# Performance work log

Measured on AMD Instinct MI355X. Metric: run time of the kernel, lower is better.

## Reference

```python
import jax, jax.numpy as jnp
import numpy as np

MIN_RANGE, MAX_RANGE = -128.0, 127.0
B, S, F_IN, F_OUT = 4, 2048, 4096, 4096
ROUNDS, FACTOR = 12, 2  # 4096 = 2**12 -> 12 prime factors of 2
NBLK = F_IN // FACTOR   # 2048 blocks of 2x2 per round


def setup_inputs() -> dict:
    key = jax.random.key(0)
    ks = jax.random.split(key, 5)
    x = jax.random.normal(ks[0], (B, S, F_IN), jnp.float32)
    weight = jax.random.normal(ks[1], (F_OUT, F_IN), jnp.float32) * (1.0 / np.sqrt(F_IN))
    bias = jax.random.normal(ks[2], (F_OUT,), jnp.float32)
    perm_keys = jax.random.split(ks[3], ROUNDS)
    permutations = jnp.stack([jax.random.permutation(k, F_IN) for k in perm_keys])  # (ROUNDS, F_IN) int32
    # random 2x2 orthogonal blocks via batched QR (stand-in for ortho_group.rvs)
    a = jax.random.normal(ks[4], (ROUNDS, NBLK, FACTOR, FACTOR), jnp.float32)
    matrices, _ = jnp.linalg.qr(a)  # (ROUNDS, NBLK, FACTOR, FACTOR)
    return {"x": x, "weight": weight, "bias": bias,
            "matrices": matrices, "permutations": permutations}


def _rotate(v, permutations, matrices):
    # v: (..., F_IN). Each round: permute features, then block-diagonal orthogonal matmul.
    for r in range(ROUNDS):
        v = v[..., permutations[r]]
        lead = v.shape[:-1]
        vb = v.reshape(lead + (NBLK, FACTOR))
        vb = jnp.einsum('kij,...kj->...ki', matrices[r], vb)
        v = vb.reshape(lead + (F_IN,))
    return v


def _quant_dequant(t):
    # per-tensor asymmetric quantization to [MIN_RANGE, MAX_RANGE] then dequant
    lo = t.min()
    hi = t.max()
    scale = (hi - lo) / (MAX_RANGE - MIN_RANGE)
    q = jnp.clip(jnp.round((t - lo) / scale) + MIN_RANGE, MIN_RANGE, MAX_RANGE)
    return (q - MIN_RANGE) * scale + lo


def reference(x, weight, bias, matrices, permutations):
    # permuted_x = permute_op(x.mT).mT  <=>  rotate along the feature (last) dim
    x_rot = _rotate(x, permutations, matrices)          # (B, S, F_IN)
    # permuted_weight = permute_op(W.mT, inv_mT).mT; for orthogonal blocks inv.mT == M
    w_rot = _rotate(weight, permutations, matrices)     # (F_OUT, F_IN)
    xq = _quant_dequant(x_rot)
    wq = _quant_dequant(w_rot)
    return jnp.einsum('bsf,of->bso', xq, wq) + bias     # (B, S, F_OUT)
```

## Files before the change

kernel.cpp:

```cpp
#include <hip/hip_runtime.h>

#define F_DIM  4096
#define NROUNDS 12
#define GM     8192
#define GN     4096
#define GK     4096
#define BK2    128
#define NIT2   (GK / BK2)

typedef int  int4v __attribute__((ext_vector_type(4)));
typedef signed char schar;

typedef __attribute__((address_space(3))) void lds_void;
typedef const __attribute__((address_space(1))) void glob_void;

__device__ __forceinline__ unsigned ordf(float f) {
    unsigned u = __float_as_uint(f);
    return (u & 0x80000000u) ? ~u : (u | 0x80000000u);
}
__device__ __forceinline__ float unordf(unsigned u) {
    unsigned v = (u & 0x80000000u) ? (u & 0x7fffffffu) : ~u;
    return __uint_as_float(v);
}

__global__ void init_mm_kernel(unsigned* mm) {
    if (threadIdx.x < 4) mm[threadIdx.x] = (threadIdx.x & 1) ? 0u : 0xFFFFFFFFu;
}

__global__ __launch_bounds__(256)
void rotate_store_kernel(const float* __restrict__ xsrc,
                         const float* __restrict__ wsrc,
                         const int*   __restrict__ perms,
                         const float* __restrict__ mats,
                         unsigned*    __restrict__ mm,
                         float*       __restrict__ xdst,
                         float*       __restrict__ wdst)
{
    __shared__ float4 buf[F_DIM];
    const int t = threadIdx.x;
    const int b = blockIdx.x;
    const bool isW = b < (GN / 4);
    const float* __restrict__ src = isW ? wsrc : xsrc;
    float* __restrict__ dst = isW ? wdst : xdst;
    unsigned* mmp = mm + (isW ? 2 : 0);
    const size_t r0 = (size_t)(isW ? b : b - GN / 4) * 4;

    const int2*   pbase = (const int2*)perms;
    const float4* mbase = (const float4*)mats;

    const float2* s0 = (const float2*)(src + (r0 + 0) * F_DIM);
    const float2* s1 = (const float2*)(src + (r0 + 1) * F_DIM);
    const float2* s2 = (const float2*)(src + (r0 + 2) * F_DIM);
    const float2* s3 = (const float2*)(src + (r0 + 3) * F_DIM);
    #pragma unroll
    for (int q = 0; q < 8; ++q) {
        const int e = t + q * 256;
        float2 a = s0[e], b2 = s1[e], c = s2[e], d = s3[e];
        buf[e]        = make_float4(a.x, b2.x, c.x, d.x);
        buf[e + 2048] = make_float4(a.y, b2.y, c.y, d.y);
    }
    __syncthreads();

    int2 pA[8], pB[8];
    float4 mA[8], mB[8];
    #pragma unroll
    for (int q = 0; q < 8; ++q) { int k = t + q * 256; pA[q] = pbase[k]; mA[q] = mbase[k]; }

    #pragma unroll 1
    for (int r = 0; r < 10; r += 2) {
        float4 va[8], vb[8];
        #pragma unroll
        for (int q = 0; q < 8; ++q) {
            int fa = pA[q].x, fb = pA[q].y;
            va[q] = buf[(fa >> 1) + ((fa & 1) << 11)];
            vb[q] = buf[(fb >> 1) + ((fb & 1) << 11)];
        }
        {
            const int2*   pr = pbase + (size_t)(r + 1) * 2048;
            const float4* mr = mbase + (size_t)(r + 1) * 2048;
            #pragma unroll
            for (int q = 0; q < 8; ++q) { int k = t + q * 256; pB[q] = pr[k]; mB[q] = mr[k]; }
        }
        __syncthreads();
        #pragma unroll
        for (int q = 0; q < 8; ++q) {
            const int k = t + q * 256;
            float4 A = va[q], B = vb[q], M = mA[q];
            buf[k]        = make_float4(M.x*A.x + M.y*B.x, M.x*A.y + M.y*B.y,
                                        M.x*A.z + M.y*B.z, M.x*A.w + M.y*B.w);
            buf[k + 2048] = make_float4(M.z*A.x + M.w*B.x, M.z*A.y + M.w*B.y,
                                        M.z*A.z + M.w*B.z, M.z*A.w + M.w*B.w);
        }
        __syncthreads();

        #pragma unroll
        for (int q = 0; q < 8; ++q) {
            int fa = pB[q].x, fb = pB[q].y;
            va[q] = buf[(fa >> 1) + ((fa & 1) << 11)];
            vb[q] = buf[(fb >> 1) + ((fb & 1) << 11)];
        }
        {
            const int2*   pr = pbase + (size_t)(r + 2) * 2048;
            const float4* mr = mbase + (size_t)(r + 2) * 2048;
            #pragma unroll
            for (int q = 0; q < 8; ++q) { int k = t + q * 256; pA[q] = pr[k]; mA[q] = mr[k]; }
        }
        __syncthreads();
        #pragma unroll
        for (int q = 0; q < 8; ++q) {
            const int k = t + q * 256;
            float4 A = va[q], B = vb[q], M = mB[q];
            buf[k]        = make_float4(M.x*A.x + M.y*B.x, M.x*A.y + M.y*B.y,
                                        M.x*A.z + M.y*B.z, M.x*A.w + M.y*B.w);
            buf[k + 2048] = make_float4(M.z*A.x + M.w*B.x, M.z*A.y + M.w*B.y,
                                        M.z*A.z + M.w*B.z, M.z*A.w + M.w*B.w);
        }
        __syncthreads();
    }

    {
        float4 va[8], vb[8];
        #pragma unroll
        for (int q = 0; q < 8; ++q) {
            int fa = pA[q].x, fb = pA[q].y;
            va[q] = buf[(fa >> 1) + ((fa & 1) << 11)];
            vb[q] = buf[(fb >> 1) + ((fb & 1) << 11)];
        }
        {
            const int2*   pr = pbase + (size_t)11 * 2048;
            const float4* mr = mbase + (size_t)11 * 2048;
            #pragma unroll
            for (int q = 0; q < 8; ++q) { int k = t + q * 256; pB[q] = pr[k]; mB[q] = mr[k]; }
        }
        __syncthreads();
        #pragma unroll
        for (int q = 0; q < 8; ++q) {
            const int k = t + q * 256;
            float4 A = va[q], B = vb[q], M = mA[q];
            buf[k]        = make_float4(M.x*A.x + M.y*B.x, M.x*A.y + M.y*B.y,
                                        M.x*A.z + M.y*B.z, M.x*A.w + M.y*B.w);
            buf[k + 2048] = make_float4(M.z*A.x + M.w*B.x, M.z*A.y + M.w*B.y,
                                        M.z*A.z + M.w*B.z, M.z*A.w + M.w*B.w);
        }
        __syncthreads();
    }

    float lmin = __FLT_MAX__, lmax = -__FLT_MAX__;
    {
        float4 va[8], vb[8];
        #pragma unroll
        for (int q = 0; q < 8; ++q) {
            int fa = pB[q].x, fb = pB[q].y;
            va[q] = buf[(fa >> 1) + ((fa & 1) << 11)];
            vb[q] = buf[(fb >> 1) + ((fb & 1) << 11)];
        }
        #pragma unroll
        for (int q = 0; q < 8; ++q) {
            const int e = t + q * 256;
            float4 A = va[q], B = vb[q], M = mB[q];
            float4 f0 = make_float4(M.x*A.x + M.y*B.x, M.x*A.y + M.y*B.y,
                                    M.x*A.z + M.y*B.z, M.x*A.w + M.y*B.w);
            float4 f1 = make_float4(M.z*A.x + M.w*B.x, M.z*A.y + M.w*B.y,
                                    M.z*A.z + M.w*B.z, M.z*A.w + M.w*B.w);
            lmin = fminf(lmin, fminf(fminf(f0.x, f0.y), fminf(f0.z, f0.w)));
            lmin = fminf(lmin, fminf(fminf(f1.x, f1.y), fminf(f1.z, f1.w)));
            lmax = fmaxf(lmax, fmaxf(fmaxf(f0.x, f0.y), fmaxf(f0.z, f0.w)));
            lmax = fmaxf(lmax, fmaxf(fmaxf(f1.x, f1.y), fmaxf(f1.z, f1.w)));
            ((float2*)(dst + (r0 + 0) * F_DIM))[e] = make_float2(f0.x, f1.x);
            ((float2*)(dst + (r0 + 1) * F_DIM))[e] = make_float2(f0.y, f1.y);
            ((float2*)(dst + (r0 + 2) * F_DIM))[e] = make_float2(f0.z, f1.z);
            ((float2*)(dst + (r0 + 3) * F_DIM))[e] = make_float2(f0.w, f1.w);
        }
    }
    #pragma unroll
    for (int off = 32; off > 0; off >>= 1) {
        lmin = fminf(lmin, __shfl_down(lmin, off));
        lmax = fmaxf(lmax, __shfl_down(lmax, off));
    }
    if ((t & 63) == 0) {
        atomicMin(&mmp[0], ordf(lmin));
        atomicMax(&mmp[1], ordf(lmax));
    }
}

__global__ __launch_bounds__(256)
void quant_row_kernel(const float* __restrict__ src,
                      schar*       __restrict__ dst,
                      int*         __restrict__ rowsum,
                      const unsigned* __restrict__ mm, int sel)
{
    const int row = blockIdx.x, t = threadIdx.x;
    const float lo = unordf(mm[sel]);
    const float hi = unordf(mm[sel + 1]);
    const float scale = (hi - lo) / 255.0f;
    const float4* s = (const float4*)(src + (size_t)row * F_DIM);
    unsigned* d = (unsigned*)(dst + (size_t)row * F_DIM);
    int sum = 0;
    #pragma unroll
    for (int j = 0; j < 4; ++j) {
        const int c = t + 256 * j;
        float4 v = s[c];
        int p0 = (int)fminf(fmaxf(rintf((v.x - lo) / scale), 0.0f), 255.0f);
        int p1 = (int)fminf(fmaxf(rintf((v.y - lo) / scale), 0.0f), 255.0f);
        int p2 = (int)fminf(fmaxf(rintf((v.z - lo) / scale), 0.0f), 255.0f);
        int p3 = (int)fminf(fmaxf(rintf((v.w - lo) / scale), 0.0f), 255.0f);
        sum += p0 + p1 + p2 + p3 - 512;
        unsigned pack = ((unsigned)(p0 - 128) & 0xffu)
                      | (((unsigned)(p1 - 128) & 0xffu) << 8)
                      | (((unsigned)(p2 - 128) & 0xffu) << 16)
                      | (((unsigned)(p3 - 128) & 0xffu) << 24);
        d[c] = pack;
    }
    #pragma unroll
    for (int off = 32; off > 0; off >>= 1) sum += __shfl_down(sum, off);
    __shared__ int part[4];
    if ((t & 63) == 0) part[t >> 6] = sum;
    __syncthreads();
    if (t == 0) rowsum[row] = part[0] + part[1] + part[2] + part[3];
}

__global__ __launch_bounds__(256)
void gemm_i8_bias_kernel(const schar* __restrict__ A,
                         const schar* __restrict__ B,
                         const float* __restrict__ bias,
                         const int*   __restrict__ Rx,
                         const int*   __restrict__ Rw,
                         const unsigned* __restrict__ mm,
                         float*       __restrict__ C)
{
    __shared__ alignas(16) schar As[128 * 8 * 16];
    __shared__ alignas(16) schar Bs[128 * 8 * 16];
    const int t = threadIdx.x;
    const int bid = blockIdx.x;
    const int mb = (bid >> 8) * 8 + (bid & 7);
    const int nb = (bid >> 3) & 31;
    const int lane = t & 63, wv = t >> 6;
    const int wm = (wv & 1) * 64, wn = (wv >> 1) * 64;
    const int rr = lane & 15, kc = lane >> 4;

    const int srow = t >> 3;
    const int cg   = (t & 7) ^ (srow & 7);
    const schar* pa = A + ((size_t)(mb * 128 + srow) * GK) + cg * 16;
    const schar* pb = B + ((size_t)(nb * 128 + srow) * GK) + cg * 16;

    int4v acc[4][4];
    const int4v zz = {0, 0, 0, 0};
    #pragma unroll
    for (int mi = 0; mi < 4; ++mi)
        #pragma unroll
        for (int ni = 0; ni < 4; ++ni)
            acc[mi][ni] = zz;

    auto stage = [&](int k0) {
        #pragma unroll
        for (int j = 0; j < 4; ++j) {
            __builtin_amdgcn_global_load_lds(
                (glob_void*)(pa + (size_t)j * 32 * GK + k0),
                (lds_void*)&As[(size_t)(wv * 64 + 256 * j) * 16], 16, 0, 0);
            __builtin_amdgcn_global_load_lds(
                (glob_void*)(pb + (size_t)j * 32 * GK + k0),
                (lds_void*)&Bs[(size_t)(wv * 64 + 256 * j) * 16], 16, 0, 0);
        }
    };

    stage(0);
    #pragma unroll 1
    for (int it = 0; it < NIT2; ++it) {
        __syncthreads();

        int4v af[2][4], bfr[2][4];
        #pragma unroll
        for (int kk = 0; kk < 2; ++kk) {
            #pragma unroll
            for (int mi = 0; mi < 4; ++mi)
                af[kk][mi] = *(const int4v*)
                    &As[(size_t)((wm + mi * 16 + rr) * 8 + ((kk * 4 + kc) ^ (rr & 7))) * 16];
            #pragma unroll
            for (int ni = 0; ni < 4; ++ni)
                bfr[kk][ni] = *(const int4v*)
                    &Bs[(size_t)((wn + ni * 16 + rr) * 8 + ((kk * 4 + kc) ^ (rr & 7))) * 16];
        }
        __syncthreads();

        if (it + 1 < NIT2) stage((it + 1) * BK2);

        #pragma unroll
        for (int kk = 0; kk < 2; ++kk)
            #pragma unroll
            for (int mi = 0; mi < 4; ++mi)
                #pragma unroll
                for (int ni = 0; ni < 4; ++ni)
                    acc[mi][ni] = __builtin_amdgcn_mfma_i32_16x16x64_i8(
                        af[kk][mi], bfr[kk][ni], acc[mi][ni], 0, 0, 0);
    }

    const float lox = unordf(mm[0]), hix = unordf(mm[1]);
    const float low = unordf(mm[2]), hiw = unordf(mm[3]);
    const float ax = (hix - lox) / 255.0f, aw = (hiw - low) / 255.0f;
    const float cx = 128.0f * ax + lox, cw = 128.0f * aw + low;
    const float sxw = ax * aw;
    const float kcc = (float)GK * cx * cw;
    const float axcw = ax * cw, awcx = aw * cx;

    float colt[4];
    #pragma unroll
    for (int ni = 0; ni < 4; ++ni) {
        const int col = nb * 128 + wn + ni * 16 + rr;
        colt[ni] = awcx * (float)Rw[col] + kcc + bias[col];
    }
    float rowt[4][4];
    #pragma unroll
    for (int mi = 0; mi < 4; ++mi)
        #pragma unroll
        for (int r = 0; r < 4; ++r)
            rowt[mi][r] = axcw * (float)Rx[mb * 128 + wm + mi * 16 + kc * 4 + r];

    #pragma unroll
    for (int mi = 0; mi < 4; ++mi) {
        #pragma unroll
        for (int ni = 0; ni < 4; ++ni) {
            const int col = nb * 128 + wn + ni * 16 + rr;
            #pragma unroll
            for (int r = 0; r < 4; ++r) {
                const int row = mb * 128 + wm + mi * 16 + kc * 4 + r;
                C[(size_t)row * GN + col] =
                    sxw * (float)acc[mi][ni][r] + rowt[mi][r] + colt[ni];
            }
        }
    }
}

extern "C" void kernel_launch(void* const* d_in, const int* in_sizes, int n_in,
                              void* d_out, int out_size, void* d_ws, size_t ws_size,
                              hipStream_t stream)
{
    (void)in_sizes; (void)n_in; (void)out_size; (void)ws_size;
    const float* x     = (const float*)d_in[0];
    const float* w     = (const float*)d_in[1];
    const float* bias  = (const float*)d_in[2];
    const float* mats  = (const float*)d_in[3];
    const int*   perms = (const int*)d_in[4];
    float* out = (float*)d_out;

    char* ws = (char*)d_ws;
    float*    wrot = (float*)ws;
    schar*    xq8  = (schar*)ws;
    int*      Rx   = (int*)(ws + (size_t)32 * 1024 * 1024);
    schar*    wq8  = (schar*)(ws + (size_t)64 * 1024 * 1024);
    int*      Rw   = (int*)(ws + (size_t)80 * 1024 * 1024);
    unsigned* mm   = (unsigned*)(ws + (size_t)81 * 1024 * 1024);
    float*    xrot = out;

    init_mm_kernel<<<1, 64, 0, stream>>>(mm);
    rotate_store_kernel<<<GN / 4 + GM / 4, 256, 0, stream>>>(
        x, w, perms, mats, mm, xrot, wrot);
    quant_row_kernel<<<GN, 256, 0, stream>>>(wrot, wq8, Rw, mm, 2);
    quant_row_kernel<<<GM, 256, 0, stream>>>(xrot, xq8, Rx, mm, 0);
    gemm_i8_bias_kernel<<<GM / 128 * GN / 128, 256, 0, stream>>>(
        xq8, wq8, bias, Rx, Rw, mm, out);
}
```

Before: 703.7 us.

## Fuse pairs of rotation rounds via precomputed composite gather metadata

A new small kernel precomputes, for each pair of rotation rounds, the four composed source indices and the selected coefficients of the first round's 2x2 blocks. The rotate kernel then applies two rounds per LDS pass: it gathers four float4 values, does two chained 2x2 mixes in registers, and stores once. This halves the number of LDS write/barrier phases, from 12 round passes to 6. It costs an extra kernel launch, more gather reads and more registers per pass, and adds a launch_bounds minimum of 2 blocks per SM.

```diff
diff --git a/kernel.cpp b/kernel.cpp
--- a/kernel.cpp
+++ b/kernel.cpp
@@ -28,10 +28,43 @@
 }
 
 __global__ __launch_bounds__(256)
+void fuse_meta_kernel(const int*   __restrict__ perms,
+                      const float* __restrict__ mats,
+                      int4v*  __restrict__ fidx,
+                      float4* __restrict__ fmaC,
+                      float4* __restrict__ fm2)
+{
+    const int g = blockIdx.x * 256 + threadIdx.x;
+    if (g >= 6 * 2048) return;
+    const int rp = g >> 11, j = g & 2047;
+    const int r0 = 2 * rp, r1 = 2 * rp + 1;
+    const int a = perms[r1 * 4096 + 2 * j];
+    const int b = perms[r1 * 4096 + 2 * j + 1];
+    const int i0 = perms[r0 * 4096 + 2 * (a >> 1)];
+    const int i1 = perms[r0 * 4096 + 2 * (a >> 1) + 1];
+    const int i2 = perms[r0 * 4096 + 2 * (b >> 1)];
+    const int i3 = perms[r0 * 4096 + 2 * (b >> 1) + 1];
+    const float4 Ma = ((const float4*)mats)[r0 * 2048 + (a >> 1)];
+    const float4 Mb = ((const float4*)mats)[r0 * 2048 + (b >> 1)];
+    float4 mc;
+    mc.x = (a & 1) ? Ma.z : Ma.x;  mc.y = (a & 1) ? Ma.w : Ma.y;
+    mc.z = (b & 1) ? Mb.z : Mb.x;  mc.w = (b & 1) ? Mb.w : Mb.y;
+    int4v s;
+    s[0] = (i0 >> 1) + ((i0 & 1) << 11);
+    s[1] = (i1 >> 1) + ((i1 & 1) << 11);
+    s[2] = (i2 >> 1) + ((i2 & 1) << 11);
+    s[3] = (i3 >> 1) + ((i3 & 1) << 11);
+    fidx[g] = s;
+    fmaC[g] = mc;
+    fm2[g]  = ((const float4*)mats)[r1 * 2048 + j];
+}
+
+__global__ __launch_bounds__(256, 2)
 void rotate_store_kernel(const float* __restrict__ xsrc,
                          const float* __restrict__ wsrc,
-                         const int*   __restrict__ perms,
-                         const float* __restrict__ mats,
+                         const int4v*  __restrict__ fidx,
+                         const float4* __restrict__ fmaC,
+                         const float4* __restrict__ fm2,
                          unsigned*    __restrict__ mm,
                          float*       __restrict__ xdst,
                          float*       __restrict__ wdst)
@@ -45,9 +78,6 @@
     unsigned* mmp = mm + (isW ? 2 : 0);
     const size_t r0 = (size_t)(isW ? b : b - GN / 4) * 4;
 
-    const int2*   pbase = (const int2*)perms;
-    const float4* mbase = (const float4*)mats;
-
     const float2* s0 = (const float2*)(src + (r0 + 0) * F_DIM);
     const float2* s1 = (const float2*)(src + (r0 + 1) * F_DIM);
     const float2* s2 = (const float2*)(src + (r0 + 2) * F_DIM);
@@ -61,116 +91,141 @@
     }
     __syncthreads();
 
-    int2 pA[8], pB[8];
-    float4 mA[8], mB[8];
-    #pragma unroll
-    for (int q = 0; q < 8; ++q) { int k = t + q * 256; pA[q] = pbase[k]; mA[q] = mbase[k]; }
+    int4v  iA[8], iB[8];
+    float4 aA[8], aB[8], mA[8], mB[8];
+    #pragma unroll
+    for (int q = 0; q < 8; ++q) {
+        int k = t + q * 256;
+        iA[q] = fidx[k]; aA[q] = fmaC[k]; mA[q] = fm2[k];
+    }
 
     #pragma unroll 1
-    for (int r = 0; r < 10; r += 2) {
-        float4 va[8], vb[8];
-        #pragma unroll
-        for (int q = 0; q < 8; ++q) {
-            int fa = pA[q].x, fb = pA[q].y;
-            va[q] = buf[(fa >> 1) + ((fa & 1) << 11)];
-            vb[q] = buf[(fb >> 1) + ((fb & 1) << 11)];
+    for (int fp = 0; fp < 4; fp += 2) {
+        float4 o0[8], o1[8];
+        #pragma unroll
+        for (int q = 0; q < 8; ++q) {
+            int4v ix = iA[q];
+            float4 A0 = buf[ix[0]], A1 = buf[ix[1]];
+            float4 B0 = buf[ix[2]], B1 = buf[ix[3]];
+            float4 ma = aA[q], m2 = mA[q];
+            float4 ca = make_float4(ma.x*A0.x + ma.y*A1.x, ma.x*A0.y + ma.y*A1.y,
+                                    ma.x*A0.z + ma.y*A1.z, ma.x*A0.w + ma.y*A1.w);
+            float4 cb = make_float4(ma.z*B0.x + ma.w*B1.x, ma.z*B0.y + ma.w*B1.y,
+                                    ma.z*B0.z + ma.w*B1.z, ma.z*B0.w + ma.w*B1.w);
+            o0[q] = make_float4(m2.x*ca.x + m2.y*cb.x, m2.x*ca.y + m2.y*cb.y,
+                                m2.x*ca.z + m2.y*cb.z, m2.x*ca.w + m2.y*cb.w);
+            o1[q] = make_float4(m2.z*ca.x + m2.w*cb.x, m2.z*ca.y + m2.w*cb.y,
+                                m2.z*ca.z + m2.w*cb.z, m2.z*ca.w + m2.w*cb.w);
         }
         {
-            const int2*   pr = pbase + (size_t)(r + 1) * 2048;
-            const float4* mr = mbase + (size_t)(r + 1) * 2048;
-            #pragma unroll
-            for (int q = 0; q < 8; ++q) { int k = t + q * 256; pB[q] = pr[k]; mB[q] = mr[k]; }
+            const size_t base = (size_t)(fp + 1) * 2048;
+            #pragma unroll
+            for (int q = 0; q < 8; ++q) {
+                size_t k = base + t + q * 256;
+                iB[q] = fidx[k]; aB[q] = fmaC[k]; mB[q] = fm2[k];
+            }
         }
         __syncthreads();
         #pragma unroll
         for (int q = 0; q < 8; ++q) {
             const int k = t + q * 256;
-            float4 A = va[q], B = vb[q], M = mA[q];
-            buf[k]        = make_float4(M.x*A.x + M.y*B.x, M.x*A.y + M.y*B.y,
-                                        M.x*A.z + M.y*B.z, M.x*A.w + M.y*B.w);
-            buf[k + 2048] = make_float4(M.z*A.x + M.w*B.x, M.z*A.y + M.w*B.y,
-                                        M.z*A.z + M.w*B.z, M.z*A.w + M.w*B.w);
-        }
-        __syncthreads();
-
-        #pragma unroll
-        for (int q = 0; q < 8; ++q) {
-            int fa = pB[q].x, fb = pB[q].y;
-            va[q] = buf[(fa >> 1) + ((fa & 1) << 11)];
-            vb[q] = buf[(fb >> 1) + ((fb & 1) << 11)];
+            buf[k]        = o0[q];
+            buf[k + 2048] = o1[q];
+        }
+        __syncthreads();
+
+        #pragma unroll
+        for (int q = 0; q < 8; ++q) {
+            int4v ix = iB[q];
+            float4 A0 = buf[ix[0]], A1 = buf[ix[1]];
+            float4 B0 = buf[ix[2]], B1 = buf[ix[3]];
+            float4 ma = aB[q], m2 = mB[q];
+            float4 ca = make_float4(ma.x*A0.x + ma.y*A1.x, ma.x*A0.y + ma.y*A1.y,
+                                    ma.x*A0.z + ma.y*A1.z, ma.x*A0.w + ma.y*A1.w);
+            float4 cb = make_float4(ma.z*B0.x + ma.w*B1.x, ma.z*B0.y + ma.w*B1.y,
+                                    ma.z*B0.z + ma.w*B1.z, ma.z*B0.w + ma.w*B1.w);
+            o0[q] = make_float4(m2.x*ca.x + m2.y*cb.x, m2.x*ca.y + m2.y*cb.y,
+                                m2.x*ca.z + m2.y*cb.z, m2.x*ca.w + m2.y*cb.w);
+            o1[q] = make_float4(m2.z*ca.x + m2.w*cb.x, m2.z*ca.y + m2.w*cb.y,
+                                m2.z*ca.z + m2.w*cb.z, m2.z*ca.w + m2.w*cb.w);
         }
         {
-            const int2*   pr = pbase + (size_t)(r + 2) * 2048;
-            const float4* mr = mbase + (size_t)(r + 2) * 2048;
-            #pragma unroll
-            for (int q = 0; q < 8; ++q) { int k = t + q * 256; pA[q] = pr[k]; mA[q] = mr[k]; }
+            const size_t base = (size_t)(fp + 2) * 2048;
+            #pragma unroll
+            for (int q = 0; q < 8; ++q) {
+                size_t k = base + t + q * 256;
+                iA[q] = fidx[k]; aA[q] = fmaC[k]; mA[q] = fm2[k];
+            }
         }
         __syncthreads();
         #pragma unroll
         for (int q = 0; q < 8; ++q) {
             const int k = t + q * 256;
-            float4 A = va[q], B = vb[q], M = mB[q];
-            buf[k]        = make_float4(M.x*A.x + M.y*B.x, M.x*A.y + M.y*B.y,
-                                        M.x*A.z + M.y*B.z, M.x*A.w + M.y*B.w);
-            buf[k + 2048] = make_float4(M.z*A.x + M.w*B.x, M.z*A.y + M.w*B.y,
-                                        M.z*A.z + M.w*B.z, M.z*A.w + M.w*B.w);
+            buf[k]        = o0[q];
+            buf[k + 2048] = o1[q];
         }
         __syncthreads();
     }
 
     {
-        float4 va[8], vb[8];
-        #pragma unroll
-        for (int q = 0; q < 8; ++q) {
-            int fa = pA[q].x, fb = pA[q].y;
-            va[q] = buf[(fa >> 1) + ((fa & 1) << 11)];
-            vb[q] = buf[(fb >> 1) + ((fb & 1) << 11)];
+        float4 o0[8], o1[8];
+        #pragma unroll
+        for (int q = 0; q < 8; ++q) {
+            int4v ix = iA[q];
+            float4 A0 = buf[ix[0]], A1 = buf[ix[1]];
+            float4 B0 = buf[ix[2]], B1 = buf[ix[3]];
+            float4 ma = aA[q], m2 = mA[q];
+            float4 ca = make_float4(ma.x*A0.x + ma.y*A1.x, ma.x*A0.y + ma.y*A1.y,
+                                    ma.x*A0.z + ma.y*A1.z, ma.x*A0.w + ma.y*A1.w);
+            float4 cb = make_float4(ma.z*B0.x + ma.w*B1.x, ma.z*B0.y + ma.w*B1.y,
+                                    ma.z*B0.z + ma.w*B1.z, ma.z*B0.w + ma.w*B1.w);
+            o0[q] = make_float4(m2.x*ca.x + m2.y*cb.x, m2.x*ca.y + m2.y*cb.y,
+                                m2.x*ca.z + m2.y*cb.z, m2.x*ca.w + m2.y*cb.w);
+            o1[q] = make_float4(m2.z*ca.x + m2.w*cb.x, m2.z*ca.y + m2.w*cb.y,
+                                m2.z*ca.z + m2.w*cb.z, m2.z*ca.w + m2.w*cb.w);
         }
         {
-            const int2*   pr = pbase + (size_t)11 * 2048;
-            const float4* mr = mbase + (size_t)11 * 2048;
-            #pragma unroll
-            for (int q = 0; q < 8; ++q) { int k = t + q * 256; pB[q] = pr[k]; mB[q] = mr[k]; }
+            const size_t base = (size_t)5 * 2048;
+            #pragma unroll
+            for (int q = 0; q < 8; ++q) {
+                size_t k = base + t + q * 256;
+                iB[q] = fidx[k]; aB[q] = fmaC[k]; mB[q] = fm2[k];
+            }
         }
         __syncthreads();
         #pragma unroll
         for (int q = 0; q < 8; ++q) {
             const int k = t + q * 256;
-            float4 A = va[q], B = vb[q], M = mA[q];
-            buf[k]        = make_float4(M.x*A.x + M.y*B.x, M.x*A.y + M.y*B.y,
-                                        M.x*A.z + M.y*B.z, M.x*A.w + M.y*B.w);
-            buf[k + 2048] = make_float4(M.z*A.x + M.w*B.x, M.z*A.y + M.w*B.y,
-                                        M.z*A.z + M.w*B.z, M.z*A.w + M.w*B.w);
+            buf[k]        = o0[q];
+            buf[k + 2048] = o1[q];
         }
         __syncthreads();
     }
 
     float lmin = __FLT_MAX__, lmax = -__FLT_MAX__;
-    {
-        float4 va[8], vb[8];
-        #pragma unroll
-        for (int q = 0; q < 8; ++q) {
-            int fa = pB[q].x, fb = pB[q].y;
-            va[q] = buf[(fa >> 1) + ((fa & 1) << 11)];
-            vb[q] = buf[(fb >> 1) + ((fb & 1) << 11)];
-        }
-        #pragma unroll
-        for (int q = 0; q < 8; ++q) {
-            const int e = t + q * 256;
-            float4 A = va[q], B = vb[q], M = mB[q];
-            float4 f0 = make_float4(M.x*A.x + M.y*B.x, M.x*A.y + M.y*B.y,
-                                    M.x*A.z + M.y*B.z, M.x*A.w + M.y*B.w);
-            float4 f1 = make_float4(M.z*A.x + M.w*B.x, M.z*A.y + M.w*B.y,
-                                    M.z*A.z + M.w*B.z, M.z*A.w + M.w*B.w);
-            lmin = fminf(lmin, fminf(fminf(f0.x, f0.y), fminf(f0.z, f0.w)));
-            lmin = fminf(lmin, fminf(fminf(f1.x, f1.y), fminf(f1.z, f1.w)));
-            lmax = fmaxf(lmax, fmaxf(fmaxf(f0.x, f0.y), fmaxf(f0.z, f0.w)));
-            lmax = fmaxf(lmax, fmaxf(fmaxf(f1.x, f1.y), fmaxf(f1.z, f1.w)));
-            ((float2*)(dst + (r0 + 0) * F_DIM))[e] = make_float2(f0.x, f1.x);
-            ((float2*)(dst + (r0 + 1) * F_DIM))[e] = make_float2(f0.y, f1.y);
-            ((float2*)(dst + (r0 + 2) * F_DIM))[e] = make_float2(f0.z, f1.z);
-            ((float2*)(dst + (r0 + 3) * F_DIM))[e] = make_float2(f0.w, f1.w);
-        }
+    #pragma unroll
+    for (int q = 0; q < 8; ++q) {
+        int4v ix = iB[q];
+        float4 A0 = buf[ix[0]], A1 = buf[ix[1]];
+        float4 B0 = buf[ix[2]], B1 = buf[ix[3]];
+        float4 ma = aB[q], m2 = mB[q];
+        float4 ca = make_float4(ma.x*A0.x + ma.y*A1.x, ma.x*A0.y + ma.y*A1.y,
+                                ma.x*A0.z + ma.y*A1.z, ma.x*A0.w + ma.y*A1.w);
+        float4 cb = make_float4(ma.z*B0.x + ma.w*B1.x, ma.z*B0.y + ma.w*B1.y,
+                                ma.z*B0.z + ma.w*B1.z, ma.z*B0.w + ma.w*B1.w);
+        float4 f0 = make_float4(m2.x*ca.x + m2.y*cb.x, m2.x*ca.y + m2.y*cb.y,
+                                m2.x*ca.z + m2.y*cb.z, m2.x*ca.w + m2.y*cb.w);
+        float4 f1 = make_float4(m2.z*ca.x + m2.w*cb.x, m2.z*ca.y + m2.w*cb.y,
+                                m2.z*ca.z + m2.w*cb.z, m2.z*ca.w + m2.w*cb.w);
+        lmin = fminf(lmin, fminf(fminf(f0.x, f0.y), fminf(f0.z, f0.w)));
+        lmin = fminf(lmin, fminf(fminf(f1.x, f1.y), fminf(f1.z, f1.w)));
+        lmax = fmaxf(lmax, fmaxf(fmaxf(f0.x, f0.y), fmaxf(f0.z, f0.w)));
+        lmax = fmaxf(lmax, fmaxf(fmaxf(f1.x, f1.y), fmaxf(f1.z, f1.w)));
+        const int e = t + q * 256;
+        ((float2*)(dst + (r0 + 0) * F_DIM))[e] = make_float2(f0.x, f1.x);
+        ((float2*)(dst + (r0 + 1) * F_DIM))[e] = make_float2(f0.y, f1.y);
+        ((float2*)(dst + (r0 + 2) * F_DIM))[e] = make_float2(f0.z, f1.z);
+        ((float2*)(dst + (r0 + 3) * F_DIM))[e] = make_float2(f0.w, f1.w);
     }
     #pragma unroll
     for (int off = 32; off > 0; off >>= 1) {
@@ -349,11 +404,15 @@
     schar*    wq8  = (schar*)(ws + (size_t)64 * 1024 * 1024);
     int*      Rw   = (int*)(ws + (size_t)80 * 1024 * 1024);
     unsigned* mm   = (unsigned*)(ws + (size_t)81 * 1024 * 1024);
+    int4v*    fidx = (int4v*)(ws + (size_t)82 * 1024 * 1024);
+    float4*   fmaC = (float4*)((char*)fidx + 6 * 2048 * sizeof(int4v));
+    float4*   fm2  = (float4*)((char*)fmaC + 6 * 2048 * sizeof(float4));
     float*    xrot = out;
 
     init_mm_kernel<<<1, 64, 0, stream>>>(mm);
+    fuse_meta_kernel<<<(6 * 2048) / 256, 256, 0, stream>>>(perms, mats, fidx, fmaC, fm2);
     rotate_store_kernel<<<GN / 4 + GM / 4, 256, 0, stream>>>(
-        x, w, perms, mats, mm, xrot, wrot);
+        x, w, fidx, fmaC, fm2, mm, xrot, wrot);
     quant_row_kernel<<<GN, 256, 0, stream>>>(wrot, wq8, Rw, mm, 2);
     quant_row_kernel<<<GM, 256, 0, stream>>>(xrot, xq8, Rx, mm, 0);
     gemm_i8_bias_kernel<<<GM / 128 * GN / 128, 256, 0, stream>>>(
```

New measurement: 752.7 us. 1.07x slower.
